# Kernel tuning notes

Measured on AMD Instinct MI355X. Metric: run time of the kernel, lower is better.

The kernel has to match this reference:

```python
import jax, jax.numpy as jnp
import numpy as np

N_NODES = 100000
N_EDGES = 500000
N_GRAPHS = 128
HID = 128          # Config.hidden_dim
KEY_EMB = HID // 4 # 32
IN_DIM = 16
FEAT_DIM = IN_DIM - 1  # key feature removed
OUT_DIM = 2
MSG_IN = 2 * HID + 1   # 257


def setup_inputs() -> dict:
    key = jax.random.key(0)
    ks = jax.random.split(key, 24)
    p = lambda k, shp: (jax.random.normal(k, shp, dtype=jnp.float32) * 0.02)
    inp = {
        "x": jax.random.normal(ks[0], (N_NODES, IN_DIM), dtype=jnp.float32),
        "W_enc": p(ks[1], (1, KEY_EMB)), "b_enc": jnp.zeros((KEY_EMB,), jnp.float32),
        "W0": p(ks[2], (FEAT_DIM + KEY_EMB, HID)), "b0": jnp.zeros((HID,), jnp.float32),
        "W1a": p(ks[3], (MSG_IN, HID)), "b1a": jnp.zeros((HID,), jnp.float32),
        "W1b": p(ks[4], (HID, HID)), "b1b": jnp.zeros((HID,), jnp.float32),
        "W2a": p(ks[5], (MSG_IN, HID)), "b2a": jnp.zeros((HID,), jnp.float32),
        "W2b": p(ks[6], (HID, HID)), "b2b": jnp.zeros((HID,), jnp.float32),
        "Wf1": p(ks[7], (4 * HID, HID)), "bf1": jnp.zeros((HID,), jnp.float32),
        "Wf2": p(ks[8], (HID, OUT_DIM)), "bf2": jnp.zeros((OUT_DIM,), jnp.float32),
        "edge_src1": jax.random.randint(ks[9], (N_EDGES,), 0, N_NODES),
        "edge_dst1": jax.random.randint(ks[10], (N_EDGES,), 0, N_NODES),
        "edge_src2": jax.random.randint(ks[11], (N_EDGES,), 0, N_NODES),
        "edge_dst2": jax.random.randint(ks[12], (N_EDGES,), 0, N_NODES),
        "batch": jnp.sort(jax.random.randint(ks[13], (N_NODES,), 0, N_GRAPHS)),
    }
    return inp


def _leaky_relu(v):
    return jnp.where(v > 0, v, 0.1 * v)


def _edge_conv(h, key_feat, src, dst, Wa, ba, Wb, bb):
    # message: [x_j - x_i, x_i, key_j - key_i] -> Linear -> LeakyReLU(0.1) -> Linear
    h_i = h[dst]                      # [E, HID] target
    h_j = h[src]                      # [E, HID] source
    m = jnp.concatenate([h_j - h_i, h_i, key_feat[src] - key_feat[dst]], axis=-1)  # [E, 257]
    m = _leaky_relu(jnp.dot(m, Wa) + ba)
    m = jnp.dot(m, Wb) + bb
    agg = jax.ops.segment_max(m, dst, num_segments=N_NODES)
    agg = jnp.where(jnp.isfinite(agg), agg, 0.0)  # nodes with no in-edges -> 0 (PyG scatter-max fill)
    return agg + h  # residual


def reference(x, W_enc, b_enc, W0, b0, W1a, b1a, W1b, b1b, W2a, b2a, W2b, b2b,
              Wf1, bf1, Wf2, bf2, edge_src1, edge_dst1, edge_src2, edge_dst2, batch):
    key_feat = x[:, 0:1]              # key_feature_idx = 0
    features = x[:, 1:]               # [N, FEAT_DIM]
    key_emb = jnp.dot(key_feat, W_enc) + b_enc  # [N, 32]
    h = jax.nn.relu(jnp.dot(jnp.concatenate([features, key_emb], axis=-1), W0) + b0)  # dropout: eval mode

    x1 = jax.nn.relu(_edge_conv(h, key_feat, edge_src1, edge_dst1, W1a, b1a, W1b, b1b))
    x2 = jax.nn.relu(_edge_conv(x1, key_feat, edge_src2, edge_dst2, W2a, b2a, W2b, b2b))

    cat = jnp.concatenate([x1, x2], axis=1)  # [N, 256]
    max_pool = jax.ops.segment_max(cat, batch, num_segments=N_GRAPHS)
    max_pool = jnp.where(jnp.isfinite(max_pool), max_pool, 0.0)
    counts = jax.ops.segment_sum(jnp.ones((N_NODES,), jnp.float32), batch, num_segments=N_GRAPHS)
    mean_pool = jax.ops.segment_sum(cat, batch, num_segments=N_GRAPHS) / jnp.maximum(counts, 1.0)[:, None]

    pooled = jnp.concatenate([max_pool, mean_pool], axis=1)  # [G, 512]
    out = jnp.dot(jax.nn.relu(jnp.dot(pooled, Wf1) + bf1), Wf2) + bf2
    return jax.nn.log_softmax(out, axis=1)
```

## Files before the change

kernel.cpp:

```cpp
#include <hip/hip_runtime.h>
#include <cstdint>

#define N_NODES 100000
#define N_EDGES 500000
#define N_GRAPHS 128
#define HID 128
#define SCANH_B ((N_NODES + 255) / 256)
#define E256_G ((N_EDGES + 255) / 256)
#define MM_G ((N_NODES + 127) / 128)
#define AH_G ((N_NODES + 511) / 512)
#define BH_G ((N_EDGES + 511) / 512)

typedef __attribute__((ext_vector_type(8))) short short8;
typedef __attribute__((ext_vector_type(4))) float f32x4;

__device__ __forceinline__ unsigned encf(float f) {
    unsigned u = __float_as_uint(f);
    return (u & 0x80000000u) ? ~u : (u | 0x80000000u);
}
__device__ __forceinline__ float decf(unsigned e) {
    unsigned u = (e & 0x80000000u) ? (e & 0x7FFFFFFFu) : ~e;
    return __uint_as_float(u);
}
__device__ __forceinline__ unsigned cvt_pk_bf16(float lo, float hi) {
    unsigned r;
    asm("v_cvt_pk_bf16_f32 %0, %1, %2" : "=v"(r) : "v"(lo), "v"(hi));
    return r;
}
__device__ __forceinline__ ushort bf16r(float f) {
    unsigned u = __float_as_uint(f);
    return (ushort)((u + 0x7fffu + ((u >> 16) & 1u)) >> 16);
}
__device__ __forceinline__ float bf2f(ushort h) {
    return __uint_as_float((unsigned)h << 16);
}

__global__ __launch_bounds__(256) void prep_hist_kernel(const float* __restrict__ W1b,
                                                        const float* __restrict__ W2b,
                                                        const float* __restrict__ W1a,
                                                        const float* __restrict__ W2a,
                                                        const float* __restrict__ W_enc,
                                                        const float* __restrict__ b_enc,
                                                        const float* __restrict__ W0,
                                                        const float* __restrict__ b0,
                                                        ushort* __restrict__ WT,
                                                        float* __restrict__ wkey,
                                                        float* __restrict__ bias0,
                                                        float* __restrict__ pooled,
                                                        const int* __restrict__ dst1,
                                                        int* __restrict__ cnt,
                                                        int* __restrict__ seq) {
    int blk = blockIdx.x;
    int tid = threadIdx.x;
    if (blk < E256_G) {
        int e = blk * 256 + tid;
        if (e < N_EDGES) seq[e] = atomicAdd(&cnt[dst1[e]], 1);
        return;
    }
    int b2 = blk - E256_G;
    if (b2 < 384) {
        int m = b2 >> 6;
        int i = (b2 & 63) * 256 + tid;
        int n = i >> 7, k = i & 127;
        int src = k * HID + n;
        float v;
        switch (m) {
            case 0: v = W1b[src]; break;
            case 1: v = W2b[src]; break;
            case 2: v = W1a[src]; break;
            case 3: v = W1a[HID * HID + src] - W1a[src]; break;
            case 4: v = W2a[src]; break;
            default: v = W2a[HID * HID + src] - W2a[src]; break;
        }
        WT[m * HID * HID + i] = bf16r(v);
        return;
    }
    if (b2 == 384) {
        if (tid < HID) {
            float wk = 0.f, bk = b0[tid];
            for (int k = 0; k < 32; ++k) {
                float w = W0[(15 + k) * HID + tid];
                wk += W_enc[k] * w;
                bk += b_enc[k] * w;
            }
            wkey[tid] = wk;
            bias0[tid] = bk;
        }
        return;
    }
    pooled[(b2 - 385) * 256 + tid] = 0.f;
}

__global__ __launch_bounds__(256) void scan_half_kernel(const int* __restrict__ cnt,
                                                        int* __restrict__ cursor,
                                                        int* __restrict__ partials) {
    __shared__ int tmp[256];
    int tid = threadIdx.x;
    int gid = blockIdx.x * 256 + tid;
    int v = (gid < N_NODES) ? cnt[gid] : 0;
    tmp[tid] = v;
    __syncthreads();
#pragma unroll
    for (int off = 1; off < 256; off <<= 1) {
        int t = (tid >= off) ? tmp[tid - off] : 0;
        __syncthreads();
        tmp[tid] += t;
        __syncthreads();
    }
    if (gid < N_NODES) cursor[gid] = tmp[tid] - v;
    if (tid == 255) partials[blockIdx.x] = tmp[255];
}

__global__ __launch_bounds__(512) void scan2_half_kernel(int* __restrict__ partials) {
    __shared__ int tmp[512];
    int tid = threadIdx.x;
    int v = (tid < SCANH_B) ? partials[tid] : 0;
    tmp[tid] = v;
    __syncthreads();
#pragma unroll
    for (int off = 1; off < 512; off <<= 1) {
        int t = (tid >= off) ? tmp[tid - off] : 0;
        __syncthreads();
        tmp[tid] += t;
        __syncthreads();
    }
    if (tid < SCANH_B) partials[tid] = tmp[tid] - v;
}

__global__ __launch_bounds__(512, 4) void build_mm_kernel(const float* __restrict__ x,
                                                          const float* __restrict__ W0,
                                                          const float* __restrict__ wkey,
                                                          const float* __restrict__ bias0,
                                                          ushort* __restrict__ h,
                                                          float* __restrict__ xkey,
                                                          const ushort* __restrict__ WuT,
                                                          const ushort* __restrict__ WvT,
                                                          const float* __restrict__ bv,
                                                          ushort* __restrict__ outu,
                                                          ushort* __restrict__ outv,
                                                          const int* __restrict__ src1,
                                                          const int* __restrict__ dst1,
                                                          const int* __restrict__ dst2,
                                                          const int* __restrict__ cnt,
                                                          const int* __restrict__ cursor,
                                                          const int* __restrict__ partials1,
                                                          int* __restrict__ cnt2w,
                                                          int* __restrict__ seq,
                                                          int* __restrict__ srcS,
                                                          int* __restrict__ dstS,
                                                          unsigned* __restrict__ agg1) {
    __shared__ ushort sH[128 * 136];
    __shared__ ushort sWT[128 * 136];
    int blk = blockIdx.x;
    int tid = threadIdx.x;

    if (blk < BH_G) {
        int e = blk * 512 + tid;
        if (e >= N_EDGES) return;
        seq[N_EDGES + e] = atomicAdd(&cnt2w[dst2[e]], 1);
        return;
    }
    int b = blk - BH_G;
    if (b >= MM_G) {
        b -= MM_G;
        if (b < AH_G) {
            int gid = b * 512 + tid;
            if (gid >= N_NODES) return;
            int c = cnt[gid];
            if (c == 0) return;
            int o = cursor[gid] + partials1[gid >> 8];
            for (int i = 0; i < c; ++i) dstS[o + i] = gid;
            bool spans = (o >> 4) != ((o + c - 1) >> 4);
            bool tail = (o + c == N_EDGES);
            if (spans || tail) {
                uint4* ap = (uint4*)(agg1 + (size_t)gid * HID);
#pragma unroll
                for (int i = 0; i < 32; ++i) ap[i] = make_uint4(0u, 0u, 0u, 0u);
            }
            return;
        }
        {
            int e = (b - AH_G) * 512 + tid;
            if (e >= N_EDGES) return;
            int idx = dst1[e];
            int pos = cursor[idx] + partials1[idx >> 8] + seq[e];
            srcS[pos] = src1[e];
            return;
        }
    }

    int n0 = b * 128;
#pragma unroll
    for (int q = 0; q < 4; ++q) {
        int c = q * 512 + tid;
        int r = c >> 4, off = (c & 15) << 3;
        int n = n0 + r;
        uint4 vv = make_uint4(0, 0, 0, 0);
        if (n < N_NODES) {
            const float* xr = x + n * 16;
            float k0 = xr[0];
            if (off == 0) xkey[n] = k0;
            float xf[15];
#pragma unroll
            for (int f = 0; f < 15; ++f) xf[f] = xr[1 + f];
            unsigned ow[4];
#pragma unroll
            for (int p = 0; p < 4; ++p) {
                int c0 = off + 2 * p;
                float a0 = bias0[c0] + k0 * wkey[c0];
                float a1 = bias0[c0 + 1] + k0 * wkey[c0 + 1];
#pragma unroll
                for (int f = 0; f < 15; ++f) {
                    float2 w2 = *(const float2*)(W0 + f * HID + c0);
                    a0 = fmaf(xf[f], w2.x, a0);
                    a1 = fmaf(xf[f], w2.y, a1);
                }
                ow[p] = cvt_pk_bf16(fmaxf(a0, 0.f), fmaxf(a1, 0.f));
            }
            vv = make_uint4(ow[0], ow[1], ow[2], ow[3]);
            *(uint4*)(h + (size_t)n * HID + off) = vv;
        }
        *(uint4*)(sH + r * 136 + off) = vv;
    }
#pragma unroll
    for (int q = 0; q < 4; ++q) {
        int c = q * 512 + tid;
        int nn = c >> 4, off = (c & 15) << 3;
        *(uint4*)(sWT + nn * 136 + off) = *(const uint4*)(WuT + nn * 128 + off);
    }
    __syncthreads();

    int lane = tid & 63, wv = tid >> 6;
    int l15 = lane & 15, quad = lane >> 4;
    int ch = wv & 1, rh = wv >> 1;

    short8 afr[2][4];
#pragma unroll
    for (int rr = 0; rr < 2; ++rr) {
        const ushort* ab = sH + (rh * 32 + rr * 16 + l15) * 136 + quad * 8;
#pragma unroll
        for (int kc = 0; kc < 4; ++kc)
            afr[rr][kc] = *(const short8*)(ab + kc * 32);
    }

#pragma unroll
    for (int pass = 0; pass < 2; ++pass) {
        ushort* out = pass ? outv : outu;
        f32x4 acc[2][4];
#pragma unroll
        for (int rr = 0; rr < 2; ++rr)
#pragma unroll
            for (int ct = 0; ct < 4; ++ct) acc[rr][ct] = (f32x4){0.f, 0.f, 0.f, 0.f};
#pragma unroll
        for (int kc = 0; kc < 4; ++kc) {
#pragma unroll
            for (int ct = 0; ct < 4; ++ct) {
                short8 bfr = *(const short8*)(sWT + ((ch * 4 + ct) * 16 + l15) * 136 + quad * 8 + kc * 32);
                acc[0][ct] = __builtin_amdgcn_mfma_f32_16x16x32_bf16(afr[0][kc], bfr, acc[0][ct], 0, 0, 0);
                acc[1][ct] = __builtin_amdgcn_mfma_f32_16x16x32_bf16(afr[1][kc], bfr, acc[1][ct], 0, 0, 0);
            }
        }
        __syncthreads();
#pragma unroll
        for (int ct = 0; ct < 4; ++ct) {
            int col = (ch * 4 + ct) * 16 + l15;
            float bb = pass ? bv[col] : 0.f;
#pragma unroll
            for (int rr = 0; rr < 2; ++rr) {
                int rowb = rh * 32 + rr * 16 + quad * 4;
                unsigned p01 = cvt_pk_bf16(acc[rr][ct][0] + bb, acc[rr][ct][1] + bb);
                unsigned p23 = cvt_pk_bf16(acc[rr][ct][2] + bb, acc[rr][ct][3] + bb);
                sH[(rowb + 0) * 136 + col] = (ushort)p01;
                sH[(rowb + 1) * 136 + col] = (ushort)(p01 >> 16);
                sH[(rowb + 2) * 136 + col] = (ushort)p23;
                sH[(rowb + 3) * 136 + col] = (ushort)(p23 >> 16);
            }
        }
        if (pass == 0) {
#pragma unroll
            for (int q = 0; q < 4; ++q) {
                int c = q * 512 + tid;
                int nn = c >> 4, off = (c & 15) << 3;
                *(uint4*)(sWT + nn * 136 + off) = *(const uint4*)(WvT + nn * 128 + off);
            }
        }
        __syncthreads();
#pragma unroll
        for (int q = 0; q < 4; ++q) {
            int c = q * 512 + tid;
            int r = c >> 4, off = (c & 15) << 3;
            int m = n0 + r;
            if (m < N_NODES)
                *(uint4*)(out + (size_t)m * HID + off) = *(const uint4*)(sH + r * 136 + off);
        }
    }
}

__global__ __launch_bounds__(512, 4) void mm2_build2_kernel(const ushort* __restrict__ in,
                                                            const unsigned* __restrict__ aggin,
                                                            const int* __restrict__ cntin,
                                                            const float* __restrict__ baddin,
                                                            ushort* __restrict__ xout,
                                                            const ushort* __restrict__ WuT,
                                                            const ushort* __restrict__ WvT,
                                                            const float* __restrict__ bv,
                                                            ushort* __restrict__ outu,
                                                            ushort* __restrict__ outv,
                                                            const int* __restrict__ src2,
                                                            const int* __restrict__ dst2,
                                                            const int* __restrict__ cnt2,
                                                            const int* __restrict__ cursor2,
                                                            const int* __restrict__ partials2,
                                                            const int* __restrict__ seq,
                                                            int* __restrict__ srcS,
                                                            int* __restrict__ dstS,
                                                            unsigned* __restrict__ agg2) {
    __shared__ ushort sH[128 * 136];
    __shared__ ushort sWT[128 * 136];
    int blk = blockIdx.x;
    int tid = threadIdx.x;

    if (blk < BH_G) {
        int e = blk * 512 + tid;
        if (e >= N_EDGES) return;
        int idx = dst2[e];
        int pos = cursor2[idx] + partials2[idx >> 8] + seq[N_EDGES + e];
        srcS[N_EDGES + pos] = src2[e];
        return;
    }
    int b = blk - BH_G;
    if (b < AH_G) {
        int gid = b * 512 + tid;
        if (gid >= N_NODES) return;
        int c = cnt2[gid];
        if (c == 0) return;
        int o = cursor2[gid] + partials2[gid >> 8];
        for (int i = 0; i < c; ++i) dstS[N_EDGES + o + i] = gid;
        bool spans = (o >> 4) != ((o + c - 1) >> 4);
        bool tail = (o + c == N_EDGES);
        if (spans || tail) {
            uint4* ap = (uint4*)(agg2 + (size_t)gid * HID);
#pragma unroll
            for (int i = 0; i < 32; ++i) ap[i] = make_uint4(0u, 0u, 0u, 0u);
        }
        return;
    }

    int n0 = (b - AH_G) * 128;
#pragma unroll
    for (int q = 0; q < 4; ++q) {
        int c = q * 512 + tid;
        int r = c >> 4, off = (c & 15) << 3;
        int n = n0 + r;
        uint4 vv = make_uint4(0, 0, 0, 0);
        if (n < N_NODES) {
            uint4 hv = *(const uint4*)(in + (size_t)n * HID + off);
            float add[8];
#pragma unroll
            for (int p = 0; p < 8; ++p) add[p] = 0.f;
            if (cntin[n] > 0) {
                uint4 e0 = *(const uint4*)(aggin + (size_t)n * HID + off);
                uint4 e1 = *(const uint4*)(aggin + (size_t)n * HID + off + 4);
                float4 bb0 = *(const float4*)(baddin + off);
                float4 bb1 = *(const float4*)(baddin + off + 4);
                add[0] = decf(e0.x) + bb0.x; add[1] = decf(e0.y) + bb0.y;
                add[2] = decf(e0.z) + bb0.z; add[3] = decf(e0.w) + bb0.w;
                add[4] = decf(e1.x) + bb1.x; add[5] = decf(e1.y) + bb1.y;
                add[6] = decf(e1.z) + bb1.z; add[7] = decf(e1.w) + bb1.w;
            }
            unsigned hw[4] = {hv.x, hv.y, hv.z, hv.w};
            unsigned ow[4];
#pragma unroll
            for (int p = 0; p < 4; ++p) {
                float lo = __uint_as_float(hw[p] << 16);
                float hi = __uint_as_float(hw[p] & 0xffff0000u);
                float r0 = fmaxf(add[2 * p] + lo, 0.f);
                float r1 = fmaxf(add[2 * p + 1] + hi, 0.f);
                ow[p] = cvt_pk_bf16(r0, r1);
            }
            vv = make_uint4(ow[0], ow[1], ow[2], ow[3]);
            *(uint4*)(xout + (size_t)n * HID + off) = vv;
        }
        *(uint4*)(sH + r * 136 + off) = vv;
    }
#pragma unroll
    for (int q = 0; q < 4; ++q) {
        int c = q * 512 + tid;
        int nn = c >> 4, off = (c & 15) << 3;
        *(uint4*)(sWT + nn * 136 + off) = *(const uint4*)(WuT + nn * 128 + off);
    }
    __syncthreads();

    int lane = tid & 63, wv = tid >> 6;
    int l15 = lane & 15, quad = lane >> 4;
    int ch = wv & 1, rh = wv >> 1;

    short8 afr[2][4];
#pragma unroll
    for (int rr = 0; rr < 2; ++rr) {
        const ushort* ab = sH + (rh * 32 + rr * 16 + l15) * 136 + quad * 8;
#pragma unroll
        for (int kc = 0; kc < 4; ++kc)
            afr[rr][kc] = *(const short8*)(ab + kc * 32);
    }

#pragma unroll
    for (int pass = 0; pass < 2; ++pass) {
        ushort* out = pass ? outv : outu;
        f32x4 acc[2][4];
#pragma unroll
        for (int rr = 0; rr < 2; ++rr)
#pragma unroll
            for (int ct = 0; ct < 4; ++ct) acc[rr][ct] = (f32x4){0.f, 0.f, 0.f, 0.f};
#pragma unroll
        for (int kc = 0; kc < 4; ++kc) {
#pragma unroll
            for (int ct = 0; ct < 4; ++ct) {
                short8 bfr = *(const short8*)(sWT + ((ch * 4 + ct) * 16 + l15) * 136 + quad * 8 + kc * 32);
                acc[0][ct] = __builtin_amdgcn_mfma_f32_16x16x32_bf16(afr[0][kc], bfr, acc[0][ct], 0, 0, 0);
                acc[1][ct] = __builtin_amdgcn_mfma_f32_16x16x32_bf16(afr[1][kc], bfr, acc[1][ct], 0, 0, 0);
            }
        }
        __syncthreads();
#pragma unroll
        for (int ct = 0; ct < 4; ++ct) {
            int col = (ch * 4 + ct) * 16 + l15;
            float bb = pass ? bv[col] : 0.f;
#pragma unroll
            for (int rr = 0; rr < 2; ++rr) {
                int rowb = rh * 32 + rr * 16 + quad * 4;
                unsigned p01 = cvt_pk_bf16(acc[rr][ct][0] + bb, acc[rr][ct][1] + bb);
                unsigned p23 = cvt_pk_bf16(acc[rr][ct][2] + bb, acc[rr][ct][3] + bb);
                sH[(rowb + 0) * 136 + col] = (ushort)p01;
                sH[(rowb + 1) * 136 + col] = (ushort)(p01 >> 16);
                sH[(rowb + 2) * 136 + col] = (ushort)p23;
                sH[(rowb + 3) * 136 + col] = (ushort)(p23 >> 16);
            }
        }
        if (pass == 0) {
#pragma unroll
            for (int q = 0; q < 4; ++q) {
                int c = q * 512 + tid;
                int nn = c >> 4, off = (c & 15) << 3;
                *(uint4*)(sWT + nn * 136 + off) = *(const uint4*)(WvT + nn * 128 + off);
            }
        }
        __syncthreads();
#pragma unroll
        for (int q = 0; q < 4; ++q) {
            int c = q * 512 + tid;
            int r = c >> 4, off = (c & 15) << 3;
            int m = n0 + r;
            if (m < N_NODES)
                *(uint4*)(out + (size_t)m * HID + off) = *(const uint4*)(sH + r * 136 + off);
        }
    }
}

__global__ __launch_bounds__(512, 6) void edge_kernel(const ushort* __restrict__ u,
                                                      const ushort* __restrict__ v,
                                                      const float* __restrict__ xkey,
                                                      const int* __restrict__ srcS,
                                                      const int* __restrict__ dstS,
                                                      const ushort* __restrict__ WbT,
                                                      const float* __restrict__ wlast,
                                                      unsigned* __restrict__ agg) {
    __shared__ ushort sWT[128 * 136];
    __shared__ ushort sU[64 * 136];
    __shared__ int sDst[64];
    __shared__ int sBnd[2];
    __shared__ unsigned sMask[3];
    int tid = threadIdx.x;

    int nwg = gridDim.x;
    int orig = blockIdx.x;
    int qq = nwg >> 3, rr8 = nwg & 7;
    int xcd = orig & 7, idx = orig >> 3;
    int wgid = (xcd < rr8 ? xcd * (qq + 1) : rr8 * (qq + 1) + (xcd - rr8) * qq) + idx;
    int w0 = wgid * 64;

#pragma unroll
    for (int q = 0; q < 4; ++q) {
        int c = q * 512 + tid;
        int n = c >> 4, off = (c & 15) << 3;
        *(uint4*)(sWT + n * 136 + off) = *(const uint4*)(WbT + n * 128 + off);
    }

    int eloc = tid >> 3;
    int sub = tid & 7;
    int kb = sub << 4;
    int lane = tid & 63, wv = tid >> 6;
    int l15 = lane & 15, quad = lane >> 4;
    int ch = wv & 1, rh = wv >> 1;

    float wreg[16];
    {
        const float4* wr4 = (const float4*)(wlast + kb);
#pragma unroll
        for (int q = 0; q < 4; ++q) {
            float4 wq = wr4[q];
            wreg[q * 4 + 0] = wq.x; wreg[q * 4 + 1] = wq.y;
            wreg[q * 4 + 2] = wq.z; wreg[q * 4 + 3] = wq.w;
        }
    }

    {
        int e = w0 + eloc;
        if (e >= N_EDGES) e = N_EDGES - 1;
        int sx = srcS[e], sy = dstS[e];
        if (sub == 0) sDst[eloc] = sy;
        if (tid < 2) {
            int eb = (tid == 0) ? (w0 - 1) : (w0 + 64);
            sBnd[tid] = (eb >= 0 && eb < N_EDGES) ? dstS[eb] : -1;
        }
        float kd = xkey[sx] - xkey[sy];
        const uint4* ur = (const uint4*)(u + (size_t)sx * HID + kb);
        const uint4* vr = (const uint4*)(v + (size_t)sy * HID + kb);
        uint4 uu[2], vvv[2];
        uu[0] = ur[0]; uu[1] = ur[1];
        vvv[0] = vr[0]; vvv[1] = vr[1];
#pragma unroll
        for (int q = 0; q < 2; ++q) {
            unsigned pu[4] = {uu[q].x, uu[q].y, uu[q].z, uu[q].w};
            unsigned pv[4] = {vvv[q].x, vvv[q].y, vvv[q].z, vvv[q].w};
            unsigned pk[4];
#pragma unroll
            for (int p = 0; p < 4; ++p) {
                float a0 = __uint_as_float(pu[p] << 16) + __uint_as_float(pv[p] << 16);
                float a1 = __uint_as_float(pu[p] & 0xffff0000u) + __uint_as_float(pv[p] & 0xffff0000u);
                a0 = fmaf(kd, wreg[q * 8 + 2 * p], a0);
                a1 = fmaf(kd, wreg[q * 8 + 2 * p + 1], a1);
                a0 = fmaxf(a0, 0.1f * a0);
                a1 = fmaxf(a1, 0.1f * a1);
                pk[p] = cvt_pk_bf16(a0, a1);
            }
            uint4 o; o.x = pk[0]; o.y = pk[1]; o.z = pk[2]; o.w = pk[3];
            *(uint4*)(sU + eloc * 136 + kb + q * 8) = o;
        }
    }
    __syncthreads();

    if (tid < 64) {
        int dprev = (tid == 0) ? sBnd[0] : sDst[tid - 1];
        unsigned long long m = __ballot(sDst[tid] != dprev);
        if (tid == 0) { sMask[0] = (unsigned)m; sMask[1] = (unsigned)(m >> 32); }
        if (tid == 63) sMask[2] = (sDst[63] != sBnd[1]) ? 1u : 0u;
    }

    short8 afr[4];
    {
        const ushort* ab = sU + (rh * 16 + l15) * 136 + quad * 8;
#pragma unroll
        for (int kc = 0; kc < 4; ++kc)
            afr[kc] = *(const short8*)(ab + kc * 32);
    }
    f32x4 acc[4];
#pragma unroll
    for (int ct = 0; ct < 4; ++ct) acc[ct] = (f32x4){0.f, 0.f, 0.f, 0.f};
#pragma unroll
    for (int kc = 0; kc < 4; ++kc) {
#pragma unroll
        for (int ct = 0; ct < 4; ++ct) {
            short8 bfr = *(const short8*)(sWT + ((ch * 4 + ct) * 16 + l15) * 136 + quad * 8 + kc * 32);
            acc[ct] = __builtin_amdgcn_mfma_f32_16x16x32_bf16(afr[kc], bfr, acc[ct], 0, 0, 0);
        }
    }
    __syncthreads();

#pragma unroll
    for (int ct = 0; ct < 4; ++ct) {
        int col = (ch * 4 + ct) * 16 + l15;
        uint2 pr;
        pr.x = cvt_pk_bf16(acc[ct][0], acc[ct][1]);
        pr.y = cvt_pk_bf16(acc[ct][2], acc[ct][3]);
        *(uint2*)(sU + col * 66 + rh * 16 + quad * 4) = pr;
    }
    __syncthreads();

    {
        int j = tid & 127;
        int q4 = tid >> 7;
        int base = q4 * 16;
        const ushort* mrow = sU + j * 66 + base;
        float vals[16];
#pragma unroll
        for (int q = 0; q < 4; ++q) {
            ushort4 mv = *(const ushort4*)(mrow + q * 4);
            vals[q * 4 + 0] = bf2f(mv.x);
            vals[q * 4 + 1] = bf2f(mv.y);
            vals[q * 4 + 2] = bf2f(mv.z);
            vals[q * 4 + 3] = bf2f(mv.w);
        }
        unsigned mlo = __builtin_amdgcn_readfirstlane(sMask[0]);
        unsigned mhi = __builtin_amdgcn_readfirstlane(sMask[1]);
        unsigned b64 = __builtin_amdgcn_readfirstlane(sMask[2]);
        unsigned long long mask = ((unsigned long long)mhi << 32) | mlo;
        unsigned slice = (unsigned)((mask >> base) & 0xFFFFull);
        unsigned nextbit = (q4 == 3) ? (b64 & 1u) : (unsigned)((mask >> (base + 16)) & 1ull);
        unsigned ext = slice | (nextbit << 16);
        bool contFrom = !(ext & 1u);
        float run = 0.f;
        bool first = true;
#pragma unroll
        for (int e3 = 0; e3 < 16; ++e3) {
            float vv2 = vals[e3];
            bool hb = (ext >> e3) & 1u;
            run = (e3 == 0 || hb) ? vv2 : fmaxf(run, vv2);
            bool end = (e3 == 15) || ((ext >> (e3 + 1)) & 1u);
            if (end) {
                int d = sDst[base + e3];
                unsigned en = encf(run);
                unsigned* ap = agg + (size_t)d * HID + j;
                bool useAtomic = (first && contFrom) || ((e3 == 15) && !nextbit);
                if (useAtomic) atomicMax(ap, en);
                else *ap = en;
                first = false;
            }
        }
    }
}

__global__ __launch_bounds__(256) void pool_kernel(const ushort* __restrict__ x1,
                                                   const unsigned* __restrict__ agg2,
                                                   const float* __restrict__ b2b,
                                                   const int* __restrict__ cnt2,
                                                   const int* __restrict__ batch,
                                                   float* __restrict__ pooled) {
    int g = blockIdx.x >> 4, s = blockIdx.x & 15;
    int tid = threadIdx.x;
    int lo = 0, hi = N_NODES;
    while (lo < hi) { int mid = (lo + hi) >> 1; if (batch[mid] < g) lo = mid + 1; else hi = mid; }
    int start = lo;
    hi = N_NODES;
    while (lo < hi) { int mid = (lo + hi) >> 1; if (batch[mid] < g + 1) lo = mid + 1; else hi = mid; }
    int end = lo;
    int cnt = end - start;
    int b0 = start + (int)((long long)cnt * s / 16);
    int b1 = start + (int)((long long)cnt * (s + 1) / 16);
    if (b1 <= b0) return;
    int j = tid & 127;
    bool isx2 = tid >= 128;
    float bbj = isx2 ? b2b[j] : 0.f;
    float mx = -INFINITY, sm = 0.f;
    for (int n = b0; n < b1; ++n) {
        float xv = bf2f(x1[(size_t)n * HID + j]);
        float vv;
        if (isx2) {
            float a = 0.f;
            if (cnt2[n] > 0) a = decf(agg2[(size_t)n * HID + j]) + bbj;
            vv = fmaxf(a + xv, 0.f);
        } else {
            vv = xv;
        }
        mx = fmaxf(mx, vv);
        sm += vv;
    }
    atomicMax((unsigned*)pooled + (size_t)g * 512 + tid, encf(mx));
    atomicAdd(pooled + (size_t)g * 512 + 256 + tid, sm);
}

__global__ __launch_bounds__(128) void final_kernel(const float* __restrict__ pooled,
                                                    const int* __restrict__ batch,
                                                    const float* __restrict__ Wf1,
                                                    const float* __restrict__ bf1,
                                                    const float* __restrict__ Wf2,
                                                    const float* __restrict__ bf2,
                                                    float* __restrict__ out) {
    __shared__ float sP[512];
    __shared__ float sH[128];
    int g = blockIdx.x, tid = threadIdx.x;
    int lo = 0, hi = N_NODES;
    while (lo < hi) { int mid = (lo + hi) >> 1; if (batch[mid] < g) lo = mid + 1; else hi = mid; }
    int start = lo;
    hi = N_NODES;
    while (lo < hi) { int mid = (lo + hi) >> 1; if (batch[mid] < g + 1) lo = mid + 1; else hi = mid; }
    int cnt = lo - start;
    float inv = 1.f / (float)(cnt > 1 ? cnt : 1);
#pragma unroll
    for (int q = 0; q < 4; ++q) {
        int idx = q * 128 + tid;
        float raw;
        if (idx < 256) {
            unsigned e = ((const unsigned*)pooled)[(size_t)g * 512 + idx];
            raw = (e == 0u) ? 0.f : decf(e);
        } else {
            raw = pooled[(size_t)g * 512 + idx] * inv;
        }
        sP[idx] = raw;
    }
    __syncthreads();
    float acc = bf1[tid];
    for (int k = 0; k < 512; ++k) acc = fmaf(sP[k], Wf1[k * HID + tid], acc);
    sH[tid] = fmaxf(acc, 0.f);
    __syncthreads();
    if (tid < 2) {
        float l = bf2[tid];
        for (int k = 0; k < 128; ++k) l = fmaf(sH[k], Wf2[k * 2 + tid], l);
        sP[tid] = l;
    }
    __syncthreads();
    if (tid == 0) {
        float l0 = sP[0], l1 = sP[1];
        float m = fmaxf(l0, l1);
        float ls = m + logf(expf(l0 - m) + expf(l1 - m));
        out[g * 2 + 0] = l0 - ls;
        out[g * 2 + 1] = l1 - ls;
    }
}

extern "C" void kernel_launch(void* const* d_in, const int* in_sizes, int n_in,
                              void* d_out, int out_size, void* d_ws, size_t ws_size,
                              hipStream_t stream) {
    const float* x     = (const float*)d_in[0];
    const float* W_enc = (const float*)d_in[1];
    const float* b_enc = (const float*)d_in[2];
    const float* W0    = (const float*)d_in[3];
    const float* b0    = (const float*)d_in[4];
    const float* W1a   = (const float*)d_in[5];
    const float* b1a   = (const float*)d_in[6];
    const float* W1b   = (const float*)d_in[7];
    const float* b1b   = (const float*)d_in[8];
    const float* W2a   = (const float*)d_in[9];
    const float* b2a   = (const float*)d_in[10];
    const float* W2b   = (const float*)d_in[11];
    const float* b2b   = (const float*)d_in[12];
    const float* Wf1   = (const float*)d_in[13];
    const float* bf1   = (const float*)d_in[14];
    const float* Wf2   = (const float*)d_in[15];
    const float* bf2   = (const float*)d_in[16];
    const int* src1    = (const int*)d_in[17];
    const int* dst1    = (const int*)d_in[18];
    const int* src2    = (const int*)d_in[19];
    const int* dst2    = (const int*)d_in[20];
    const int* batch   = (const int*)d_in[21];

    const size_t NB = (size_t)N_NODES * HID;
    ushort* hbuf  = (ushort*)d_ws;
    unsigned* agg1 = (unsigned*)(hbuf + NB);
    unsigned* agg2 = agg1 + NB;
    ushort* ubuf  = (ushort*)(agg2 + NB);
    ushort* vbuf  = ubuf + NB;
    ushort* WT    = vbuf + NB;
    ushort* WbT1 = WT;
    ushort* WbT2 = WT + 1 * HID * HID;
    ushort* WuT1 = WT + 2 * HID * HID;
    ushort* WvT1 = WT + 3 * HID * HID;
    ushort* WuT2 = WT + 4 * HID * HID;
    ushort* WvT2 = WT + 5 * HID * HID;
    float* wkey  = (float*)(WT + 6 * HID * HID);
    float* bias0 = wkey + 128;
    float* xkey  = bias0 + 128;
    float* pooled = xkey + N_NODES;
    int* cnt    = (int*)(pooled + 128 * 512);
    int* cursor = cnt + 2 * N_NODES;
    int* partials1 = cursor + 2 * N_NODES;
    int* partials2 = partials1 + 512;
    int* srcS = partials2 + 512;
    int* dstS = srcS + 2 * N_EDGES;
    int* seq  = dstS + 2 * N_EDGES;

    const int edgeGrid = (N_EDGES + 63) / 64;
    const int prepGrid = E256_G + 385 + 256;
    const int buildMmGrid = BH_G + MM_G + AH_G + BH_G;
    const int mm2Grid = BH_G + AH_G + MM_G;

    hipMemsetAsync(cnt, 0, 2 * N_NODES * sizeof(int), stream);
    prep_hist_kernel<<<prepGrid, 256, 0, stream>>>(W1b, W2b, W1a, W2a, W_enc, b_enc, W0, b0,
                                                   WT, wkey, bias0, pooled, dst1, cnt, seq);
    scan_half_kernel<<<SCANH_B, 256, 0, stream>>>(cnt, cursor, partials1);
    scan2_half_kernel<<<1, 512, 0, stream>>>(partials1);

    build_mm_kernel<<<buildMmGrid, 512, 0, stream>>>(x, W0, wkey, bias0, hbuf, xkey,
                                                     WuT1, WvT1, b1a, ubuf, vbuf,
                                                     src1, dst1, dst2, cnt, cursor, partials1,
                                                     cnt + N_NODES, seq, srcS, dstS, agg1);

    scan_half_kernel<<<SCANH_B, 256, 0, stream>>>(cnt + N_NODES, cursor + N_NODES, partials2);
    scan2_half_kernel<<<1, 512, 0, stream>>>(partials2);

    edge_kernel<<<edgeGrid, 512, 0, stream>>>(ubuf, vbuf, xkey, srcS, dstS, WbT1,
                                              W1a + 256 * HID, agg1);

    mm2_build2_kernel<<<mm2Grid, 512, 0, stream>>>(hbuf, agg1, cnt, b1b, hbuf,
                                                   WuT2, WvT2, b2a, ubuf, vbuf,
                                                   src2, dst2, cnt + N_NODES, cursor + N_NODES,
                                                   partials2, seq, srcS, dstS, agg2);
    edge_kernel<<<edgeGrid, 512, 0, stream>>>(ubuf, vbuf, xkey, srcS + N_EDGES, dstS + N_EDGES,
                                              WbT2, W2a + 256 * HID, agg2);

    pool_kernel<<<N_GRAPHS * 16, 256, 0, stream>>>(hbuf, agg2, b2b, cnt + N_NODES, batch, pooled);
    final_kernel<<<N_GRAPHS, 128, 0, stream>>>(pooled, batch, Wf1, bf1, Wf2, bf2, (float*)d_out);
}
```

Before: 442.4 us.

## Move layer-2 destination histogram from build_mm into first edge kernel

The atomic histogram over dst2 edges is moved out of build_mm_kernel and into the first edge_kernel launch, where it runs as every ninth block interleaved with the edge-message blocks. The layer-2 scan launches are placed after this edge kernel so they still see complete counts. The aim is to shorten the critical build_mm launch and hide the histogram atomics under the heavier edge work. The cost is extra blocks in edge_kernel, a modulo-based remapping of block indices, and possible contention between histogram atomics and the agg atomics.

```diff
diff --git a/kernel.cpp b/kernel.cpp
--- a/kernel.cpp
+++ b/kernel.cpp
@@ -10,6 +10,7 @@
 #define MM_G ((N_NODES + 127) / 128)
 #define AH_G ((N_NODES + 511) / 512)
 #define BH_G ((N_EDGES + 511) / 512)
+#define EDGE_G ((N_EDGES + 63) / 64)
 
 typedef __attribute__((ext_vector_type(8))) short short8;
 typedef __attribute__((ext_vector_type(4))) float f32x4;
@@ -140,12 +141,10 @@
                                                           ushort* __restrict__ outv,
                                                           const int* __restrict__ src1,
                                                           const int* __restrict__ dst1,
-                                                          const int* __restrict__ dst2,
                                                           const int* __restrict__ cnt,
                                                           const int* __restrict__ cursor,
                                                           const int* __restrict__ partials1,
-                                                          int* __restrict__ cnt2w,
-                                                          int* __restrict__ seq,
+                                                          const int* __restrict__ seq,
                                                           int* __restrict__ srcS,
                                                           int* __restrict__ dstS,
                                                           unsigned* __restrict__ agg1) {
@@ -154,17 +153,10 @@
     int blk = blockIdx.x;
     int tid = threadIdx.x;
 
-    if (blk < BH_G) {
-        int e = blk * 512 + tid;
-        if (e >= N_EDGES) return;
-        seq[N_EDGES + e] = atomicAdd(&cnt2w[dst2[e]], 1);
-        return;
-    }
-    int b = blk - BH_G;
-    if (b >= MM_G) {
-        b -= MM_G;
-        if (b < AH_G) {
-            int gid = b * 512 + tid;
+    if (blk >= MM_G) {
+        int zb = blk - MM_G;
+        if (zb < AH_G) {
+            int gid = zb * 512 + tid;
             if (gid >= N_NODES) return;
             int c = cnt[gid];
             if (c == 0) return;
@@ -180,7 +172,7 @@
             return;
         }
         {
-            int e = (b - AH_G) * 512 + tid;
+            int e = (zb - AH_G) * 512 + tid;
             if (e >= N_EDGES) return;
             int idx = dst1[e];
             int pos = cursor[idx] + partials1[idx >> 8] + seq[e];
@@ -189,7 +181,7 @@
         }
     }
 
-    int n0 = b * 128;
+    int n0 = blk * 128;
 #pragma unroll
     for (int q = 0; q < 4; ++q) {
         int c = q * 512 + tid;
@@ -464,7 +456,11 @@
                                                       const int* __restrict__ dstS,
                                                       const ushort* __restrict__ WbT,
                                                       const float* __restrict__ wlast,
-                                                      unsigned* __restrict__ agg) {
+                                                      unsigned* __restrict__ agg,
+                                                      const int* __restrict__ dst2h,
+                                                      int* __restrict__ cnt2w,
+                                                      int* __restrict__ seqh,
+                                                      int histN) {
     __shared__ ushort sWT[128 * 136];
     __shared__ ushort sU[64 * 136];
     __shared__ int sDst[64];
@@ -472,10 +468,23 @@
     __shared__ unsigned sMask[3];
     int tid = threadIdx.x;
 
-    int nwg = gridDim.x;
-    int orig = blockIdx.x;
+    int wg;
+    if (histN) {
+        int r9 = blockIdx.x % 9, q9 = blockIdx.x / 9;
+        if (r9 == 0) {
+            int e = q9 * 512 + tid;
+            if (e < N_EDGES) seqh[e] = atomicAdd(&cnt2w[dst2h[e]], 1);
+            return;
+        }
+        wg = q9 * 8 + (r9 - 1);
+        if (wg >= EDGE_G) return;
+    } else {
+        wg = blockIdx.x;
+    }
+
+    const int nwg = EDGE_G;
     int qq = nwg >> 3, rr8 = nwg & 7;
-    int xcd = orig & 7, idx = orig >> 3;
+    int xcd = wg & 7, idx = wg >> 3;
     int wgid = (xcd < rr8 ? xcd * (qq + 1) : rr8 * (qq + 1) + (xcd - rr8) * qq) + idx;
     int w0 = wgid * 64;
 
@@ -759,10 +768,10 @@
     int* dstS = srcS + 2 * N_EDGES;
     int* seq  = dstS + 2 * N_EDGES;
 
-    const int edgeGrid = (N_EDGES + 63) / 64;
     const int prepGrid = E256_G + 385 + 256;
-    const int buildMmGrid = BH_G + MM_G + AH_G + BH_G;
+    const int buildMmGrid = MM_G + AH_G + BH_G;
     const int mm2Grid = BH_G + AH_G + MM_G;
+    const int edge1Grid = EDGE_G + BH_G;
 
     hipMemsetAsync(cnt, 0, 2 * N_NODES * sizeof(int), stream);
     prep_hist_kernel<<<prepGrid, 256, 0, stream>>>(W1b, W2b, W1a, W2a, W_enc, b_enc, W0, b0,
@@ -772,21 +781,23 @@
 
     build_mm_kernel<<<buildMmGrid, 512, 0, stream>>>(x, W0, wkey, bias0, hbuf, xkey,
                                                      WuT1, WvT1, b1a, ubuf, vbuf,
-                                                     src1, dst1, dst2, cnt, cursor, partials1,
-                                                     cnt + N_NODES, seq, srcS, dstS, agg1);
+                                                     src1, dst1, cnt, cursor, partials1,
+                                                     seq, srcS, dstS, agg1);
+
+    edge_kernel<<<edge1Grid, 512, 0, stream>>>(ubuf, vbuf, xkey, srcS, dstS, WbT1,
+                                               W1a + 256 * HID, agg1,
+                                               dst2, cnt + N_NODES, seq + N_EDGES, 1);
 
     scan_half_kernel<<<SCANH_B, 256, 0, stream>>>(cnt + N_NODES, cursor + N_NODES, partials2);
     scan2_half_kernel<<<1, 512, 0, stream>>>(partials2);
-
-    edge_kernel<<<edgeGrid, 512, 0, stream>>>(ubuf, vbuf, xkey, srcS, dstS, WbT1,
-                                              W1a + 256 * HID, agg1);
 
     mm2_build2_kernel<<<mm2Grid, 512, 0, stream>>>(hbuf, agg1, cnt, b1b, hbuf,
                                                    WuT2, WvT2, b2a, ubuf, vbuf,
                                                    src2, dst2, cnt + N_NODES, cursor + N_NODES,
                                                    partials2, seq, srcS, dstS, agg2);
-    edge_kernel<<<edgeGrid, 512, 0, stream>>>(ubuf, vbuf, xkey, srcS + N_EDGES, dstS + N_EDGES,
-                                              WbT2, W2a + 256 * HID, agg2);
+    edge_kernel<<<EDGE_G, 512, 0, stream>>>(ubuf, vbuf, xkey, srcS + N_EDGES, dstS + N_EDGES,
+                                            WbT2, W2a + 256 * HID, agg2,
+                                            nullptr, nullptr, nullptr, 0);
 
     pool_kernel<<<N_GRAPHS * 16, 256, 0, stream>>>(hbuf, agg2, b2b, cnt + N_NODES, batch, pooled);
     final_kernel<<<N_GRAPHS, 128, 0, stream>>>(pooled, batch, Wf1, bf1, Wf2, bf2, (float*)d_out);
```

After: 439.2 us. About the same (-0.7%).
